# Kernel optimization log

Measured on AMD Instinct MI355X. Metric: run time of the kernel, lower is better.

Reference implementation:

```python
import jax, jax.numpy as jnp
import numpy as np

B, C, H, W = 4, 8, 240, 240      # batch, feature planes, image size
P, S, O, K = 10, 5, 15, 7        # patchsize, stride, nl_match_window, k neighbors
F = 64                           # embed cnn hidden features
EPS = 1e-5
NEG = -1e9


def _conv(x, w, b=None):
    y = jax.lax.conv_general_dilated(x, w, (1, 1), 'SAME',
                                     dimension_numbers=('NCHW', 'OIHW', 'NCHW'))
    return y if b is None else y + b[None, :, None, None]


def _bn(x, g, b, m, v):
    # inference-mode batchnorm
    s = g * jax.lax.rsqrt(v + EPS)
    return x * s[None, :, None, None] + (b - m * s)[None, :, None, None]


def _cnn(x, w1, g1, b1, m1, v1, w2, g2, b2, m2, v2, w3, c3):
    # conv-bn-relu, conv-bn-relu, conv(+bias): depth=3 embedding cnn
    h = jax.nn.relu(_bn(_conv(x, w1), g1, b1, m1, v1))
    h = jax.nn.relu(_bn(_conv(h, w2), g2, b2, m2, v2))
    return _conv(h, w3, c3)


def _im2patch(x):
    # [B,c,H,W] -> ([B, g*g, c*P*P], g); patch grid g x g with stride S
    b, c, hh, _ = x.shape
    g = (hh - P) // S + 1
    r = (jnp.arange(g) * S)[:, None] + jnp.arange(P)               # [g,P]
    p = x[:, :, r[:, None, :, None], r[None, :, None, :]]         # [B,c,g,g,P,P]
    return p.transpose(0, 2, 3, 1, 4, 5).reshape(b, g * g, c * P * P), g


def _neighbor_index(g):
    # O x O window of patch-grid candidates around each query patch, clamped at borders
    start = np.clip(np.arange(g) - O // 2, 0, g - O)               # [g]
    win = start[:, None] + np.arange(O)                            # [g,O]
    I = (win[:, None, :, None] * g + win[None, :, None, :]).reshape(g * g, O * O)
    mask = I == np.arange(g * g)[:, None]                          # exclude_self
    return jnp.asarray(I), jnp.asarray(mask)


def _n3block(x, ep, tp):
    b = x.shape[0]
    xe = _cnn(x, *ep)                      # embedding [B,8,H,W]; ye = xe
    log_t = _cnn(x, *tp)                   # external temperature map [B,1,H,W]
    xe_p, g = _im2patch(xe)                # [B,M,800]
    yg_p, _ = _im2patch(x)                 # data patches [B,M,800]
    lt_p, _ = _im2patch(log_t)             # [B,M,100]
    lt = jnp.mean(lt_p, axis=-1)           # per-patch log temperature [B,M]
    I, self_mask = _neighbor_index(g)
    M, O2 = I.shape
    ynorm = jnp.sum(xe_p * xe_p, axis=-1)  # [B,M]

    # squared euclidean distances to the O2 window candidates, one offset at a time
    @jax.checkpoint
    def dcontrib(c):
        idx = I[:, c]                                              # [M]
        y = xe_p[:, idx, :]                                        # [B,M,800]
        return ynorm[:, idx] - 2.0 * jnp.einsum('bmd,bmd->bm', xe_p, y)

    _, Dt = jax.lax.scan(lambda carry, c: (carry, dcontrib(c)), 0, jnp.arange(O2))
    D = ynorm[:, :, None] + jnp.moveaxis(Dt, 0, -1)                # [B,M,O2]

    # continuous relaxation of k-NN selection (N3: repeated softmax + log1p update)
    logits = -D * jnp.exp(-lt)[:, :, None]
    logits = jnp.where(self_mask[None], NEG, logits)
    ws = []
    for _ in range(K):
        w = jax.nn.softmax(logits, axis=-1)
        ws.append(w)
        logits = logits + jnp.log1p(-jnp.clip(w, 0.0, 1.0 - 1e-6))
    Wk = jnp.stack(ws, axis=2)                                     # [B,M,K,O2]

    # temperature-weighted aggregation of data patches
    Dg = yg_p.shape[-1]

    @jax.checkpoint
    def acontrib(c):
        idx = I[:, c]
        return Wk[:, :, :, c][..., None] * yg_p[:, idx, :][:, :, None, :]

    z0 = jnp.zeros((b, M, K, Dg), x.dtype)
    z, _ = jax.lax.scan(lambda acc, c: (acc + acontrib(c), 0), z0, jnp.arange(O2))

    # fold overlapping patches back to image (average over overlaps)
    z = z.reshape(b, g, g, K, C, P, P).transpose(0, 3, 4, 1, 2, 5, 6)
    z = z.reshape(b, K * C, g, g, P, P)
    r = (jnp.arange(g) * S)[:, None] + jnp.arange(P)
    Rb = jnp.broadcast_to(r[:, None, :, None], (g, g, P, P))
    Cb = jnp.broadcast_to(r[None, :, None, :], (g, g, P, P))
    out = jnp.zeros((b, K * C, H, W), x.dtype).at[:, :, Rb, Cb].add(z)
    cnt = jnp.zeros((H, W), x.dtype).at[Rb, Cb].add(1.0)
    return jnp.concatenate([x, out / cnt[None, None]], axis=1)     # [B,(K+1)*C,H,W]


def setup_inputs() -> dict:
    key = jax.random.key(0)
    ks = jax.random.split(key, 16)

    def cw(k, o, i):
        return jax.random.normal(k, (o, i, 3, 3), jnp.float32) / np.float32(np.sqrt(9.0 * i))

    def bnp(k, c):
        k1, k2, k3, k4 = jax.random.split(k, 4)
        g = jax.random.uniform(k1, (c,), jnp.float32, 0.5, 1.5)
        be = 0.1 * jax.random.normal(k2, (c,), jnp.float32)
        m = 0.1 * jax.random.normal(k3, (c,), jnp.float32)
        v = jax.random.uniform(k4, (c,), jnp.float32, 0.5, 1.5)
        return g, be, m, v

    e_g1, e_b1, e_m1, e_v1 = bnp(ks[3], F)
    e_g2, e_b2, e_m2, e_v2 = bnp(ks[4], F)
    t_g1, t_b1, t_m1, t_v1 = bnp(ks[5], F)
    t_g2, t_b2, t_m2, t_v2 = bnp(ks[6], F)
    return dict(
        x=jax.random.normal(ks[0], (B, C, H, W), jnp.float32),
        e_w1=cw(ks[1], F, C), e_g1=e_g1, e_b1=e_b1, e_m1=e_m1, e_v1=e_v1,
        e_w2=cw(ks[2], F, F), e_g2=e_g2, e_b2=e_b2, e_m2=e_m2, e_v2=e_v2,
        e_w3=cw(ks[7], C, F), e_c3=0.1 * jax.random.normal(ks[8], (C,), jnp.float32),
        t_w1=cw(ks[9], F, C), t_g1=t_g1, t_b1=t_b1, t_m1=t_m1, t_v1=t_v1,
        t_w2=cw(ks[10], F, F), t_g2=t_g2, t_b2=t_b2, t_m2=t_m2, t_v2=t_v2,
        t_w3=cw(ks[11], 1, F), t_c3=0.1 * jax.random.normal(ks[12], (1,), jnp.float32),
    )


def reference(x, e_w1, e_g1, e_b1, e_m1, e_v1, e_w2, e_g2, e_b2, e_m2, e_v2, e_w3, e_c3,
              t_w1, t_g1, t_b1, t_m1, t_v1, t_w2, t_g2, t_b2, t_m2, t_v2, t_w3, t_c3):
    ep = (e_w1, e_g1, e_b1, e_m1, e_v1, e_w2, e_g2, e_b2, e_m2, e_v2, e_w3, e_c3)
    tp = (t_w1, t_g1, t_b1, t_m1, t_v1, t_w2, t_g2, t_b2, t_m2, t_v2, t_w3, t_c3)
    return _n3block(x, ep, tp)
```

## Files before the change

kernel.cpp:

```cpp
#include <hip/hip_runtime.h>
#include <hip/hip_bf16.h>

using bf16 = __hip_bfloat16;
typedef __attribute__((ext_vector_type(8))) short s8v;
typedef __attribute__((ext_vector_type(4))) float f4v;
#define DEVINL __device__ __forceinline__

constexpr int B_ = 4, C_ = 8, H_ = 240, W_ = 240;
constexpr int P_ = 10, S_ = 5, K_ = 7;
constexpr int G_ = 47, M_ = G_ * G_, O2_ = 225, D_ = 800;
constexpr int HW_ = H_ * W_;
constexpr int NC_ = 48;
constexpr int ND_ = 16;
constexpr int ASTR_ = NC_ * ND_ * 7;
constexpr int CFSTR_ = 3 * 7 * 2 * 512;
constexpr size_t CTSZ_ = (size_t)B_ * 48 * 15 * 2304;

DEVINL float loadf(const void* p, size_t i, int isf32) {
  return isf32 ? ((const float*)p)[i] : __bfloat162float(((const bf16*)p)[i]);
}
DEVINL int wsg(int g) { int s = g - 7; if (s < 0) s = 0; if (s > G_ - 15) s = G_ - 15; return s; }
DEVINL ushort bf16rn(float x) {
  uint u = __float_as_uint(x);
  return (ushort)((u + 0x7FFF + ((u >> 16) & 1)) >> 16);
}

DEVINL float bredsum(float v, float* red, int t) {
#pragma unroll
  for (int off = 32; off; off >>= 1) v += __shfl_xor(v, off);
  __syncthreads();
  if ((t & 63) == 0) red[t >> 6] = v;
  __syncthreads();
  return red[0] + red[1] + red[2] + red[3];
}

__global__ __launch_bounds__(256) void detect_k(const ushort* __restrict__ xr, int* __restrict__ flag) {
  __shared__ int red[4];
  const int t = threadIdx.x;
  int wild = 0;
  for (int i = t; i < 8192; i += 256) {
    const ushort u = xr[2 * i];
    const int ex = (u >> 7) & 0xFF;
    if (ex == 0xFF || ex > 130 || (ex != 0 && ex < 100)) ++wild;
  }
#pragma unroll
  for (int off = 32; off; off >>= 1) wild += __shfl_xor(wild, off);
  __syncthreads();
  if ((t & 63) == 0) red[t >> 6] = wild;
  __syncthreads();
  if (t == 0) flag[0] = (red[0] + red[1] + red[2] + red[3] > 2048) ? 1 : 0;
}

__global__ __launch_bounds__(256) void cvt_x_k(const void* __restrict__ x, const int* __restrict__ flag,
                                               float* __restrict__ xf) {
  const int i = blockIdx.x * 256 + threadIdx.x;
  xf[i] = loadf(x, i, flag[0]);
}

__global__ __launch_bounds__(256) void cvt2_k(const float* __restrict__ xf, float* __restrict__ xfc) {
  const int pg = blockIdx.x * 256 + threadIdx.x;
  const int b = pg / HW_, pix = pg % HW_;
  float v[8];
#pragma unroll
  for (int ch = 0; ch < 8; ++ch) v[ch] = xf[((size_t)(b * 8 + ch)) * HW_ + pix];
  float4* dst = reinterpret_cast<float4*>(xfc + (size_t)pg * 8);
  dst[0] = make_float4(v[0], v[1], v[2], v[3]);
  dst[1] = make_float4(v[4], v[5], v[6], v[7]);
}

template<int CIN, int COUT, bool BN>
__global__ __launch_bounds__(256) void prep_k(
    const void* __restrict__ w, const void* __restrict__ p1, const void* __restrict__ p2,
    const void* __restrict__ p3, const void* __restrict__ p4,
    float* __restrict__ wf, float* __restrict__ bfv, const int* __restrict__ flag)
{
  const int f = flag[0];
  const int idx = blockIdx.x * 256 + threadIdx.x;
  if (idx < CIN * 9 * COUT) {
    const int oc = idx % COUT, r = idx / COUT, tap = r % 9, ci = r / 9;
    float s = 1.f;
    if (BN) s = loadf(p1, oc, f) * rsqrtf(loadf(p4, oc, f) + 1e-5f);
    wf[idx] = loadf(w, ((size_t)oc * CIN + ci) * 9 + tap, f) * s;
  }
  if (idx < COUT) {
    float bb;
    if (BN) { float s = loadf(p1, idx, f) * rsqrtf(loadf(p4, idx, f) + 1e-5f); bb = loadf(p2, idx, f) - loadf(p3, idx, f) * s; }
    else bb = loadf(p1, idx, f);
    bfv[idx] = bb;
  }
}

__global__ __launch_bounds__(256) void wprep2_k(
    const void* __restrict__ w, const void* __restrict__ p1, const void* __restrict__ p4,
    ushort* __restrict__ wfr, const int* __restrict__ flag)
{
  const int f = flag[0];
  const int idx = blockIdx.x * 256 + threadIdx.x;
  if (idx >= 4608) return;
  const int l = idx & 63, ks = (idx >> 6) % 18, g = idx / 1152;
  const int tap = ks >> 1, s = ks & 1, lg = (l >> 4) & 3, ln = l & 15;
  const int oc = 16 * g + ln;
  const float sc = loadf(p1, oc, f) * rsqrtf(loadf(p4, oc, f) + 1e-5f);
#pragma unroll
  for (int e = 0; e < 8; ++e) {
    const int ci = 32 * s + 8 * lg + e;
    const float wv = loadf(w, ((size_t)oc * 64 + ci) * 9 + tap, f) * sc;
    const ushort hb = bf16rn(wv);
    const float hf = __uint_as_float(((uint)hb) << 16);
    const ushort lb = bf16rn(wv - hf);
    wfr[(((size_t)(g * 18 + ks) * 2 + 0) * 64 + l) * 8 + e] = hb;
    wfr[(((size_t)(g * 18 + ks) * 2 + 1) * 64 + l) * 8 + e] = lb;
  }
}

__global__ __launch_bounds__(256, 3) void conv12_k(
    const float* __restrict__ xf, const float* __restrict__ wf1,
    const float* __restrict__ b1, const ushort* __restrict__ wfr2,
    const float* __restrict__ b2, float* __restrict__ out)
{
  __shared__ short smem[2 * 13056];
  float* raw_s = (float*)smem;
  short* c1h = smem;
  short* c1l = smem + 13056;
  const int b = blockIdx.z;
  const int r0 = blockIdx.y * 4, c0 = blockIdx.x * 32;
  const int t = threadIdx.x;
  for (int i = t; i < 8 * 8 * 36; i += 256) {
    const int col = i % 36, rem = i / 36, ci = rem & 7, row = rem >> 3;
    const int gr = r0 - 2 + row, gc = c0 - 2 + col;
    float v = 0.f;
    if (gr >= 0 && gr < H_ && gc >= 0 && gc < W_)
      v = xf[(((size_t)b * C_ + ci) * H_ + gr) * W_ + gc];
    raw_s[i] = v;
  }
  __syncthreads();
  {
    const int w = t >> 6;
    const int h = __builtin_amdgcn_readfirstlane(w & 1);
    const int ps0 = (t & 63) + ((w >> 1) << 6);
    const float* __restrict__ wb = wf1 + 32 * h;
    float a1[2][32];
#pragma unroll
    for (int j = 0; j < 2; ++j)
#pragma unroll
      for (int o = 0; o < 32; ++o) a1[j][o] = 0.f;
    int qv[2], uv[2]; bool pok[2];
#pragma unroll
    for (int j = 0; j < 2; ++j) {
      int p = ps0 + 128 * j;
      pok[j] = p < 204;
      if (!pok[j]) p = 0;
      qv[j] = p / 34; uv[j] = p % 34;
    }
#pragma unroll 1
    for (int ct = 0; ct < 72; ++ct) {
      const int tap = ct % 9, dy = tap / 3, dx = tap % 3;
      float4 w4[8];
#pragma unroll
      for (int o4 = 0; o4 < 8; ++o4)
        w4[o4] = *reinterpret_cast<const float4*>(wb + ct * 64 + 4 * o4);
      const int ci = ct / 9;
#pragma unroll
      for (int j = 0; j < 2; ++j) {
        const float v = raw_s[((qv[j] + dy) * 8 + ci) * 36 + uv[j] + dx];
#pragma unroll
        for (int o4 = 0; o4 < 8; ++o4) {
          a1[j][4*o4+0] = fmaf(v, w4[o4].x, a1[j][4*o4+0]);
          a1[j][4*o4+1] = fmaf(v, w4[o4].y, a1[j][4*o4+1]);
          a1[j][4*o4+2] = fmaf(v, w4[o4].z, a1[j][4*o4+2]);
          a1[j][4*o4+3] = fmaf(v, w4[o4].w, a1[j][4*o4+3]);
        }
      }
    }
    __syncthreads();
#pragma unroll
    for (int j = 0; j < 2; ++j) {
      if (pok[j]) {
        const int gr1 = r0 - 1 + qv[j], gc1 = c0 - 1 + uv[j];
        const bool inimg = (gr1 >= 0 && gr1 < H_ && gc1 >= 0 && gc1 < W_);
#pragma unroll
        for (int jb = 0; jb < 4; ++jb) {
          s8v vh, vl;
#pragma unroll
          for (int e = 0; e < 8; ++e) {
            const int o = 8 * jb + e;
            float a = fmaxf(a1[j][o] + b1[32 * h + o], 0.f);
            if (!inimg) a = 0.f;
            const ushort hb = bf16rn(a);
            const float hf = __uint_as_float(((uint)hb) << 16);
            const ushort lb = bf16rn(a - hf);
            vh[e] = (short)hb; vl[e] = (short)lb;
          }
          const int idx = ((qv[j] * 8 + 4 * h + jb) * 34 + uv[j]) * 8;
          *reinterpret_cast<s8v*>(c1h + idx) = vh;
          *reinterpret_cast<s8v*>(c1l + idx) = vl;
        }
      }
    }
  }
  __syncthreads();
  const int l = t & 63;
  const int g = __builtin_amdgcn_readfirstlane(t >> 6);
  const int lg = (l >> 4) & 3, ln = l & 15;
  const int lanebase = (lg * 34 + ln) * 8;
  f4v acc[4][2];
#pragma unroll
  for (int rr = 0; rr < 4; ++rr)
#pragma unroll
    for (int tt = 0; tt < 2; ++tt) acc[rr][tt] = (f4v){0.f, 0.f, 0.f, 0.f};
#pragma unroll
  for (int tt = 0; tt < 2; ++tt)
#pragma unroll
    for (int s = 0; s < 2; ++s)
#pragma unroll
      for (int dc = 0; dc < 3; ++dc) {
        s8v Ah[3], Al[3];
#pragma unroll
        for (int dr = 0; dr < 3; ++dr) {
          const int ks = (3 * dr + dc) * 2 + s;
          Ah[dr] = *reinterpret_cast<const s8v*>(wfr2 + (((size_t)(g * 18 + ks) * 2 + 0) * 64 + l) * 8);
          Al[dr] = *reinterpret_cast<const s8v*>(wfr2 + (((size_t)(g * 18 + ks) * 2 + 1) * 64 + l) * 8);
        }
        s8v Bf[6];
#pragma unroll
        for (int row = 0; row < 6; ++row)
          Bf[row] = *reinterpret_cast<const s8v*>(c1h + ((row * 8 + 4 * s) * 34 + tt * 16 + dc) * 8 + lanebase);
#pragma unroll
        for (int dr = 0; dr < 3; ++dr)
#pragma unroll
          for (int rr = 0; rr < 4; ++rr) {
            acc[rr][tt] = __builtin_amdgcn_mfma_f32_16x16x32_bf16(Ah[dr], Bf[rr + dr], acc[rr][tt], 0, 0, 0);
            acc[rr][tt] = __builtin_amdgcn_mfma_f32_16x16x32_bf16(Al[dr], Bf[rr + dr], acc[rr][tt], 0, 0, 0);
          }
#pragma unroll
        for (int row = 0; row < 6; ++row)
          Bf[row] = *reinterpret_cast<const s8v*>(c1l + ((row * 8 + 4 * s) * 34 + tt * 16 + dc) * 8 + lanebase);
#pragma unroll
        for (int dr = 0; dr < 3; ++dr)
#pragma unroll
          for (int rr = 0; rr < 4; ++rr)
            acc[rr][tt] = __builtin_amdgcn_mfma_f32_16x16x32_bf16(Ah[dr], Bf[rr + dr], acc[rr][tt], 0, 0, 0);
      }
  float b2r[4];
#pragma unroll
  for (int reg = 0; reg < 4; ++reg) b2r[reg] = b2[16 * g + 4 * lg + reg];
#pragma unroll
  for (int rr = 0; rr < 4; ++rr)
#pragma unroll
    for (int tt = 0; tt < 2; ++tt) {
      const int col = c0 + tt * 16 + ln;
      if (col < W_) {
#pragma unroll
        for (int reg = 0; reg < 4; ++reg) {
          const int oc = 16 * g + 4 * lg + reg;
          out[(((size_t)b * 64 + oc) * H_ + r0 + rr) * W_ + col] = fmaxf(acc[rr][tt][reg] + b2r[reg], 0.f);
        }
      }
    }
}

template<int CIN, int COUT, bool RELU>
__global__ __launch_bounds__(256) void conv3x3_k(
    const float* __restrict__ in, const float* __restrict__ wf,
    const float* __restrict__ bias, float* __restrict__ out)
{
  constexpr int CC = 8;
  __shared__ float in_s[CC][18][18];
  const int b = blockIdx.z;
  const int x0 = blockIdx.x * 16, y0 = blockIdx.y * 16;
  const int t = threadIdx.x, tx = t & 15, ty = t >> 4;
  float acc[COUT];
#pragma unroll
  for (int i = 0; i < COUT; ++i) acc[i] = 0.f;
  for (int ch = 0; ch < CIN / CC; ++ch) {
    __syncthreads();
    for (int idx = t; idx < CC * 324; idx += 256) {
      const int cil = idx / 324, rr = (idx % 324) / 18, cc = idx % 18;
      const int gr = y0 + rr - 1, gc = x0 + cc - 1;
      float v = 0.f;
      if (gr >= 0 && gr < H_ && gc >= 0 && gc < W_)
        v = in[(((size_t)b * CIN + ch * CC + cil) * H_ + gr) * W_ + gc];
      in_s[cil][rr][cc] = v;
    }
    __syncthreads();
#pragma unroll 1
    for (int cil = 0; cil < CC; ++cil) {
      float v[9];
#pragma unroll
      for (int dy = 0; dy < 3; ++dy)
#pragma unroll
        for (int dx = 0; dx < 3; ++dx)
          v[dy * 3 + dx] = in_s[cil][ty + dy][tx + dx];
      const float* wrow = wf + (size_t)(ch * CC + cil) * 9 * COUT;
#pragma unroll
      for (int tap = 0; tap < 9; ++tap)
#pragma unroll
        for (int oc = 0; oc < COUT; ++oc)
          acc[oc] = fmaf(v[tap], wrow[tap * COUT + oc], acc[oc]);
    }
  }
  const int orow = y0 + ty, ocol = x0 + tx;
#pragma unroll
  for (int oc = 0; oc < COUT; ++oc) {
    float r = acc[oc] + bias[oc];
    if (RELU) r = fmaxf(r, 0.f);
    out[(((size_t)b * COUT + oc) * H_ + orow) * W_ + ocol] = r;
  }
}

__global__ __launch_bounds__(256) void patch_stats_k(
    const float* __restrict__ xe, const float* __restrict__ logt,
    float* __restrict__ ynorm, float* __restrict__ tfac)
{
  __shared__ float red[4];
  const int m = blockIdx.x, b = blockIdx.y, t = threadIdx.x;
  const int gi = m / G_, gj = m % G_;
  const int r0 = gi * S_, c0 = gj * S_;
  float s = 0.f;
  for (int d = t; d < D_; d += 256) {
    const int chn = d / 100, rem = d % 100, pi = rem / 10, pj = rem % 10;
    const float v = xe[(((size_t)b * C_ + chn) * H_ + r0 + pi) * W_ + c0 + pj];
    s += v * v;
  }
  float l = 0.f;
  if (t < 100) l = logt[((size_t)b * H_ + r0 + t / 10) * W_ + c0 + t % 10];
  s = bredsum(s, red, t);
  l = bredsum(l, red, t);
  if (t == 0) { ynorm[b * M_ + m] = s; tfac[b * M_ + m] = expf(-l * 0.01f); }
}

__global__ __launch_bounds__(256) void cellprep_k(const float* __restrict__ xe, ushort* __restrict__ cf) {
  const int ci = blockIdx.x, b = blockIdx.y, t = threadIdx.x;
  const size_t base = ((size_t)(b * 48) + ci) * CFSTR_;
  for (int idx = t; idx < 48 * 224; idx += 256) {
    const int cj = idx / 224, k = idx % 224;
    const int ks = k >> 5, r32 = k & 31, lg = r32 >> 3, e = r32 & 7;
    const int chunk = cj >> 4, ln = cj & 15;
    float v = 0.f;
    if (k < 200) {
      const int ch = k / 25, r25 = k % 25, rp = r25 / 5, cp = r25 % 5;
      v = xe[(((size_t)b * C_ + ch) * H_ + ci * 5 + rp) * W_ + cj * 5 + cp];
    }
    const ushort hb = bf16rn(v);
    const float hf = __uint_as_float(((uint)hb) << 16);
    const ushort lb = bf16rn(v - hf);
    const int l = lg * 16 + ln;
    const size_t o = base + ((size_t)((chunk * 7 + ks) * 2) * 64 + l) * 8 + e;
    cf[o] = hb;
    cf[o + 512] = lb;
  }
}

__global__ __launch_bounds__(192) void gram_k(const ushort* __restrict__ cf, float* __restrict__ Ct) {
  const int blk = blockIdx.x, b = blockIdx.y;
  const int ci = blk / 3, CA = blk % 3;
  const int t = threadIdx.x, l = t & 63;
  const int CB = __builtin_amdgcn_readfirstlane(t >> 6);
  const int lg = (l >> 4) & 3, ln = l & 15;
  const size_t cbase = ((size_t)(b * 48) + ci) * CFSTR_;
  s8v A[14];
#pragma unroll
  for (int ks = 0; ks < 7; ++ks)
#pragma unroll
    for (int hl = 0; hl < 2; ++hl)
      A[ks * 2 + hl] = *reinterpret_cast<const s8v*>(cf + cbase + ((size_t)((CA * 7 + ks) * 2 + hl) * 64 + l) * 8);
  const int dimax = min(14, 47 - ci);
#pragma unroll 1
  for (int di = 0; di <= dimax; ++di) {
    const size_t bbase = cbase + (size_t)di * CFSTR_;
    f4v acc = (f4v){0.f, 0.f, 0.f, 0.f};
#pragma unroll
    for (int ks = 0; ks < 7; ++ks) {
      const s8v Bh = *reinterpret_cast<const s8v*>(cf + bbase + ((size_t)((CB * 7 + ks) * 2 + 0) * 64 + l) * 8);
      const s8v Bl = *reinterpret_cast<const s8v*>(cf + bbase + ((size_t)((CB * 7 + ks) * 2 + 1) * 64 + l) * 8);
      acc = __builtin_amdgcn_mfma_f32_16x16x32_bf16(A[2 * ks], Bh, acc, 0, 0, 0);
      acc = __builtin_amdgcn_mfma_f32_16x16x32_bf16(A[2 * ks + 1], Bh, acc, 0, 0, 0);
      acc = __builtin_amdgcn_mfma_f32_16x16x32_bf16(A[2 * ks], Bl, acc, 0, 0, 0);
      acc = __builtin_amdgcn_mfma_f32_16x16x32_bf16(A[2 * ks + 1], Bl, acc, 0, 0, 0);
    }
    float* __restrict__ Co = Ct + ((size_t)(b * 48 + ci) * 15 + di) * 2304;
#pragma unroll
    for (int reg = 0; reg < 4; ++reg) {
      const int i = CA * 16 + 4 * lg + reg;
      Co[i * 48 + CB * 16 + ln] = acc[reg];
    }
  }
}

__global__ __launch_bounds__(256) void dist6_k(
    const float* __restrict__ Ct, const float* __restrict__ ynorm,
    const float* __restrict__ tfac, float* __restrict__ Wk)
{
  __shared__ float red[16][17];
  const int tile = blockIdx.x, b = blockIdx.y, t = threadIdx.x;
  const int gi = tile / 3, qj0 = (tile % 3) * 16;
  const int q = t & 15, ni = t >> 4;
  const int nic = (ni < 15) ? ni : 14;
  const int wr0 = wsg(gi);
  const int qj = qj0 + q;
  const bool qok = (qj < G_);
  const int qjc = qok ? qj : G_ - 1;
  const bool act = qok && (ni < 15);
  const int m = gi * G_ + qjc;
  const float ynq = ynorm[b * M_ + m];
  const float tfq = tfac[b * M_ + m];
  const int nr = wr0 + nic;
  const int di = nr - gi;
  const int sgj = wsg(qjc);
  constexpr size_t SLAB = 15 * 2304;
  float logit[15];
#pragma unroll
  for (int dj = 0; dj < 15; ++dj) {
    const int nc = sgj + dj;
    const int nm = nr * G_ + nc;
    const float* p0;
    if (di >= 0)
      p0 = Ct + ((size_t)(b * 48 + gi) * 15 + di) * 2304 + qjc * 48 + nc;
    else
      p0 = Ct + ((size_t)(b * 48 + nr) * 15 + (-di)) * 2304 + nc * 48 + qjc;
    const float dot = p0[0] + p0[49] + p0[SLAB] + p0[SLAB + 49];
    const float Dv = ynq + ynorm[b * M_ + nm] - 2.f * dot;
    logit[dj] = (nm == m) ? -1e9f : -Dv * tfq;
    if (!act) logit[dj] = -3.0e38f;
  }
  const size_t wkb = ((size_t)(b * M_ + m) * K_) * O2_ + nic * 15;
#pragma unroll 1
  for (int k = 0; k < K_; ++k) {
    float pm = -3.0e38f;
#pragma unroll
    for (int dj = 0; dj < 15; ++dj) pm = fmaxf(pm, logit[dj]);
    red[q][ni] = pm;
    __syncthreads();
    float gm = red[q][0];
#pragma unroll
    for (int i = 1; i < 16; ++i) gm = fmaxf(gm, red[q][i]);
    __syncthreads();
    float e[15]; float es = 0.f;
#pragma unroll
    for (int dj = 0; dj < 15; ++dj) { e[dj] = act ? expf(logit[dj] - gm) : 0.f; es += e[dj]; }
    red[q][ni] = es;
    __syncthreads();
    float tot = red[q][0];
#pragma unroll
    for (int i = 1; i < 16; ++i) tot += red[q][i];
    __syncthreads();
    const float inv = 1.f / tot;
#pragma unroll
    for (int dj = 0; dj < 15; ++dj) {
      const float w = e[dj] * inv;
      if (act) Wk[wkb + (size_t)k * O2_ + dj] = w;
      logit[dj] += log1pf(-fminf(w, 1.f - 1e-6f));
    }
  }
}

__global__ __launch_bounds__(256) void atab_k(const float* __restrict__ Wk, float* __restrict__ A) {
  const int cell = blockIdx.x, b = blockIdx.y, t = threadIdx.x;
  const int ci = cell / NC_, cj = cell % NC_;
  const int di = t >> 4, dj = t & 15;
  const int gi0 = max(ci - 1, 0), gi1 = min(ci, G_ - 1);
  const int gj0 = max(cj - 1, 0), gj1 = min(cj, G_ - 1);
  const int oi0 = wsg(gi0) - gi0, oi1 = wsg(gi1) - gi1;
  const int oj0 = wsg(gj0) - gj0, oj1 = wsg(gj1) - gj1;
  const int bi = min(oi0, oi1), bj = min(oj0, oj1);
  const int wi0 = bi + di - oi0, wi1 = bi + di - oi1;
  const int wj0 = bj + dj - oj0, wj1 = bj + dj - oj1;
  const bool vi0 = (wi0 >= 0 && wi0 < 15);
  const bool vi1 = (gi1 != gi0) && (wi1 >= 0 && wi1 < 15);
  const bool vj0 = (wj0 >= 0 && wj0 < 15);
  const bool vj1 = (gj1 != gj0) && (wj1 >= 0 && wj1 < 15);
  const size_t Wb = (size_t)b * M_ * K_ * O2_;
  const size_t Ab = ((((size_t)(b * NC_ + ci)) * ND_ + di) * NC_ + cj) * ND_ * 7 + dj * 7;
#pragma unroll 1
  for (int k = 0; k < K_; ++k) {
    float s = 0.f;
    if (vi0 && vj0) s += Wk[Wb + ((size_t)(gi0 * G_ + gj0) * K_ + k) * O2_ + wi0 * 15 + wj0];
    if (vi0 && vj1) s += Wk[Wb + ((size_t)(gi0 * G_ + gj1) * K_ + k) * O2_ + wi0 * 15 + wj1];
    if (vi1 && vj0) s += Wk[Wb + ((size_t)(gi1 * G_ + gj0) * K_ + k) * O2_ + wi1 * 15 + wj0];
    if (vi1 && vj1) s += Wk[Wb + ((size_t)(gi1 * G_ + gj1) * K_ + k) * O2_ + wi1 * 15 + wj1];
    A[Ab + k] = s;
  }
}

__global__ __launch_bounds__(256, 3) void agg3_k(
    const float* __restrict__ xf, const float* __restrict__ xfc,
    const float* __restrict__ A, void* __restrict__ out, const int* __restrict__ flag)
{
  __shared__ float a_s[8448];
  const int b = blockIdx.y, t = threadIdx.x;
  const int i = blockIdx.x;
  const int xcd = i & 7, slot = i >> 3;
  const int ci = (slot / 5) * 8 + xcd;
  const int r = ci * 5 + slot % 5;
  const int gi0 = max(ci - 1, 0), gi1 = min(ci, G_ - 1);
  const int bi = min(wsg(gi0) - gi0, wsg(gi1) - gi1);
  const int c = t;
  const int cj = (c < W_) ? c / 5 : NC_ - 1;
  const int gj0 = max(cj - 1, 0), gj1 = min(cj, G_ - 1);
  const int bj = min(wsg(gj0) - gj0, wsg(gj1) - gj1);
  const int cbase = c + 5 * bj;
  int dst[21];
#pragma unroll
  for (int j = 0; j < 21; ++j) {
    const int idx = t + 256 * j;
    const int cjj = idx / 112, rem = idx % 112, dj = rem / 7, kk = rem % 7;
    dst[j] = cjj * 132 + dj * 8 + kk;
  }
  float acc[C_][K_];
#pragma unroll
  for (int ch = 0; ch < C_; ++ch)
#pragma unroll
    for (int k = 0; k < K_; ++k) acc[ch][k] = 0.f;
  const size_t Aslab = (((size_t)(b * NC_ + ci)) * ND_) * ASTR_;
  const float* __restrict__ xcb = xfc + (size_t)b * HW_ * 8;
#pragma unroll 1
  for (int di = 0; di < ND_; ++di) {
    __syncthreads();
    const float* __restrict__ Ag = A + Aslab + (size_t)di * ASTR_ + t;
#pragma unroll
    for (int j = 0; j < 21; ++j)
      a_s[dst[j]] = Ag[256 * j];
    __syncthreads();
    int rp = r + 5 * (bi + di);
    rp = min(max(rp, 0), H_ - 1);
    const float* __restrict__ xrow = xcb + (size_t)rp * (W_ * 8);
    const float* __restrict__ arow = a_s + cj * 132;
#pragma unroll 1
    for (int dj = 0; dj < ND_; ++dj) {
      int cp = cbase + 5 * dj;
      cp = min(max(cp, 0), W_ - 1);
      const float4 x0 = *reinterpret_cast<const float4*>(xrow + cp * 8);
      const float4 x1 = *reinterpret_cast<const float4*>(xrow + cp * 8 + 4);
      const float4 a0 = *reinterpret_cast<const float4*>(arow + dj * 8);
      const float4 a1 = *reinterpret_cast<const float4*>(arow + dj * 8 + 4);
      const float xv[8] = {x0.x, x0.y, x0.z, x0.w, x1.x, x1.y, x1.z, x1.w};
      const float av[7] = {a0.x, a0.y, a0.z, a0.w, a1.x, a1.y, a1.z};
#pragma unroll
      for (int ch = 0; ch < C_; ++ch)
#pragma unroll
        for (int k = 0; k < K_; ++k) acc[ch][k] = fmaf(xv[ch], av[k], acc[ch][k]);
    }
  }
  if (c < W_) {
    const float inv = 1.f / (((r >= S_ && r <= 234) ? 2.f : 1.f) * ((c >= S_ && c <= 234) ? 2.f : 1.f));
    const int isf = flag[0];
    const size_t pix = (size_t)r * W_ + c;
    const float* __restrict__ xb = xf + (size_t)b * C_ * HW_;
#pragma unroll
    for (int ch = 0; ch < C_; ++ch) {
      const float v = xb[(size_t)ch * HW_ + pix];
      const size_t o = ((size_t)b * 64 + ch) * HW_ + pix;
      if (isf) ((float*)out)[o] = v; else ((bf16*)out)[o] = __float2bfloat16(v);
    }
#pragma unroll
    for (int k = 0; k < K_; ++k)
#pragma unroll
      for (int ch = 0; ch < C_; ++ch) {
        const float v = acc[ch][k] * inv;
        const size_t o = ((size_t)b * 64 + 8 + k * C_ + ch) * HW_ + pix;
        if (isf) ((float*)out)[o] = v; else ((bf16*)out)[o] = __float2bfloat16(v);
      }
  }
}

extern "C" void kernel_launch(void* const* d_in, const int* in_sizes, int n_in,
                              void* d_out, int out_size, void* d_ws, size_t ws_size,
                              hipStream_t stream) {
  const void* x = d_in[0];

  float* ws = (float*)d_ws;
  const size_t nH = (size_t)B_ * 64 * HW_;
  const size_t nXE = (size_t)B_ * C_ * HW_;
  const size_t nLT = (size_t)B_ * HW_;
  const size_t nYN = (size_t)B_ * M_;
  size_t off = 0;
  int*   flag  = (int*)(ws + off); off += 4;
  float* xf    = ws + off; off += nXE;
  float* h1    = ws + off; off += nH;
  float* h2    = ws + off; off += nH;
  float* xe    = ws + off; off += nXE;
  float* logt  = ws + off; off += nLT;
  float* ynorm = ws + off; off += nYN;
  float* tfac  = ws + off; off += nYN;
  float* wf1e = ws + off; off += 8 * 9 * 64;
  float* wf2e = ws + off; off += 64 * 9 * 64;
  float* wf3e = ws + off; off += 64 * 9 * 8;
  float* wf1t = ws + off; off += 8 * 9 * 64;
  float* wf2t = ws + off; off += 64 * 9 * 64;
  float* wf3t = ws + off; off += 64 * 9 * 1;
  float* bf1e = ws + off; off += 64;
  float* bf2e = ws + off; off += 64;
  float* bf3e = ws + off; off += 8;
  float* bf1t = ws + off; off += 64;
  float* bf2t = ws + off; off += 64;
  float* bf3t = ws + off; off += 1;
  ushort* wfr2e = (ushort*)(ws + off); off += 36864;
  ushort* wfr2t = (ushort*)(ws + off); off += 36864;
  float* Wk   = h1;
  float* Ctab = h2;
  ushort* cellfrag = (ushort*)(h2 + CTSZ_);
  float* Atab = h2;
  float* xfc  = h1;

  detect_k<<<1, 256, 0, stream>>>((const ushort*)x, flag);
  cvt_x_k<<<nXE / 256, 256, 0, stream>>>(x, flag, xf);

  prep_k<8, 64, true ><<<18, 256, 0, stream>>>(d_in[1], d_in[2], d_in[3], d_in[4], d_in[5], wf1e, bf1e, flag);
  prep_k<64, 64, true ><<<144, 256, 0, stream>>>(d_in[6], d_in[7], d_in[8], d_in[9], d_in[10], wf2e, bf2e, flag);
  prep_k<64, 8, false><<<18, 256, 0, stream>>>(d_in[11], d_in[12], nullptr, nullptr, nullptr, wf3e, bf3e, flag);
  prep_k<8, 64, true ><<<18, 256, 0, stream>>>(d_in[13], d_in[14], d_in[15], d_in[16], d_in[17], wf1t, bf1t, flag);
  prep_k<64, 64, true ><<<144, 256, 0, stream>>>(d_in[18], d_in[19], d_in[20], d_in[21], d_in[22], wf2t, bf2t, flag);
  prep_k<64, 1, false><<<3, 256, 0, stream>>>(d_in[23], d_in[24], nullptr, nullptr, nullptr, wf3t, bf3t, flag);
  wprep2_k<<<18, 256, 0, stream>>>(d_in[6], d_in[7], d_in[10], wfr2e, flag);
  wprep2_k<<<18, 256, 0, stream>>>(d_in[18], d_in[19], d_in[22], wfr2t, flag);

  const dim3 gcv(8, 60, B_);
  const dim3 g16(15, 15, B_);
  conv12_k<<<gcv, 256, 0, stream>>>(xf, wf1e, bf1e, wfr2e, bf2e, h2);
  conv3x3_k<64, 8, false><<<g16, 256, 0, stream>>>(h2, wf3e, bf3e, xe);
  conv12_k<<<gcv, 256, 0, stream>>>(xf, wf1t, bf1t, wfr2t, bf2t, h1);
  conv3x3_k<64, 1, false><<<g16, 256, 0, stream>>>(h1, wf3t, bf3t, logt);

  patch_stats_k<<<dim3(M_, B_), 256, 0, stream>>>(xe, logt, ynorm, tfac);
  cellprep_k<<<dim3(48, B_), 256, 0, stream>>>(xe, cellfrag);
  gram_k<<<dim3(144, B_), 192, 0, stream>>>(cellfrag, Ctab);
  dist6_k<<<dim3(G_ * 3, B_), 256, 0, stream>>>(Ctab, ynorm, tfac, Wk);

  atab_k<<<dim3(NC_ * NC_, B_), 256, 0, stream>>>(Wk, Atab);
  cvt2_k<<<(B_ * HW_) / 256, 256, 0, stream>>>(xf, xfc);
  agg3_k<<<dim3(H_, B_), 256, 0, stream>>>(xf, xfc, Atab, d_out, flag);
}
```

Measured before the change: 794.2 us.

## Merge embed and temperature conv12 launches; register-prefetch A tiles in aggregation

The two conv12 launches (embedding CNN and temperature CNN) become one launch with a doubled z grid, where blockIdx.z selects the network's weights and output buffer. This removes a launch and lets both networks' blocks fill the GPU together. Separately, the aggregation kernel now loads the next di slab of A into registers while the current slab is used, overlapping global loads with the FMA loop. That costs 21 extra registers per thread, which may reduce occupancy.

```diff
diff --git a/kernel.cpp b/kernel.cpp
--- a/kernel.cpp
+++ b/kernel.cpp
@@ -114,15 +114,24 @@
 }
 
 __global__ __launch_bounds__(256, 3) void conv12_k(
-    const float* __restrict__ xf, const float* __restrict__ wf1,
-    const float* __restrict__ b1, const ushort* __restrict__ wfr2,
-    const float* __restrict__ b2, float* __restrict__ out)
+    const float* __restrict__ xf,
+    const float* __restrict__ wf1e, const float* __restrict__ b1e,
+    const ushort* __restrict__ wfr2e, const float* __restrict__ b2e,
+    const float* __restrict__ wf1t, const float* __restrict__ b1t,
+    const ushort* __restrict__ wfr2t, const float* __restrict__ b2t,
+    float* __restrict__ oute, float* __restrict__ outt)
 {
   __shared__ short smem[2 * 13056];
   float* raw_s = (float*)smem;
   short* c1h = smem;
   short* c1l = smem + 13056;
-  const int b = blockIdx.z;
+  const int z = blockIdx.z;
+  const int b = z & 3, net = z >> 2;
+  const float* __restrict__ wf1 = net ? wf1t : wf1e;
+  const float* __restrict__ b1 = net ? b1t : b1e;
+  const ushort* __restrict__ wfr2 = net ? wfr2t : wfr2e;
+  const float* __restrict__ b2 = net ? b2t : b2e;
+  float* __restrict__ out = net ? outt : oute;
   const int r0 = blockIdx.y * 4, c0 = blockIdx.x * 32;
   const int t = threadIdx.x;
   for (int i = t; i < 8 * 8 * 36; i += 256) {
@@ -513,14 +522,23 @@
     for (int k = 0; k < K_; ++k) acc[ch][k] = 0.f;
   const size_t Aslab = (((size_t)(b * NC_ + ci)) * ND_) * ASTR_;
   const float* __restrict__ xcb = xfc + (size_t)b * HW_ * 8;
+  float rg[21];
+  {
+    const float* __restrict__ Ag = A + Aslab + t;
+#pragma unroll
+    for (int j = 0; j < 21; ++j) rg[j] = Ag[256 * j];
+  }
 #pragma unroll 1
   for (int di = 0; di < ND_; ++di) {
     __syncthreads();
-    const float* __restrict__ Ag = A + Aslab + (size_t)di * ASTR_ + t;
-#pragma unroll
-    for (int j = 0; j < 21; ++j)
-      a_s[dst[j]] = Ag[256 * j];
-    __syncthreads();
+#pragma unroll
+    for (int j = 0; j < 21; ++j) a_s[dst[j]] = rg[j];
+    __syncthreads();
+    if (di + 1 < ND_) {
+      const float* __restrict__ Agn = A + Aslab + (size_t)(di + 1) * ASTR_ + t;
+#pragma unroll
+      for (int j = 0; j < 21; ++j) rg[j] = Agn[256 * j];
+    }
     int rp = r + 5 * (bi + di);
     rp = min(max(rp, 0), H_ - 1);
     const float* __restrict__ xrow = xcb + (size_t)rp * (W_ * 8);
@@ -614,11 +632,11 @@
   wprep2_k<<<18, 256, 0, stream>>>(d_in[6], d_in[7], d_in[10], wfr2e, flag);
   wprep2_k<<<18, 256, 0, stream>>>(d_in[18], d_in[19], d_in[22], wfr2t, flag);
 
-  const dim3 gcv(8, 60, B_);
+  const dim3 gcv(8, 60, 2 * B_);
   const dim3 g16(15, 15, B_);
-  conv12_k<<<gcv, 256, 0, stream>>>(xf, wf1e, bf1e, wfr2e, bf2e, h2);
+  conv12_k<<<gcv, 256, 0, stream>>>(xf, wf1e, bf1e, wfr2e, bf2e,
+                                    wf1t, bf1t, wfr2t, bf2t, h2, h1);
   conv3x3_k<64, 8, false><<<g16, 256, 0, stream>>>(h2, wf3e, bf3e, xe);
-  conv12_k<<<gcv, 256, 0, stream>>>(xf, wf1t, bf1t, wfr2t, bf2t, h1);
   conv3x3_k<64, 1, false><<<g16, 256, 0, stream>>>(h1, wf3t, bf3t, logt);
 
   patch_stats_k<<<dim3(M_, B_), 256, 0, stream>>>(xe, logt, ynorm, tfac);
```

After: 826.1 us. 1.04x slower.
